# Kernel tuning notes

Measured on AMD Instinct MI355X. Metric: run time of the kernel, lower is better.

Reference implementation:

```python
import jax, jax.numpy as jnp
import numpy as np

D = 4096
B_BITS = 4
NUM_CENTROIDS = 2 ** B_BITS  # 16 uniform centroids in [-1, 1]
N_TOKENS = 8192


def setup_inputs() -> dict:
    key = jax.random.key(0)
    kx, kp = jax.random.split(key)
    x = jax.random.normal(kx, (N_TOKENS, D), dtype=jnp.float32)
    # Orthogonal rotation Pi via QR of a random Gaussian (matches torch.linalg.qr)
    rand_mat = jax.random.normal(kp, (D, D), dtype=jnp.float32)
    Pi, _ = jnp.linalg.qr(rand_mat)
    centroids = jnp.linspace(-1.0, 1.0, NUM_CENTROIDS, dtype=jnp.float32)
    return {"x": x, "Pi": Pi, "centroids": centroids}


def _quantize(y, centroids):
    # Centroids are uniformly spaced on [-1, 1]; nearest-centroid argmin has the
    # closed form below (identical result to the broadcast |y - c| argmin, without
    # materializing the O(N*d*2^b) distance tensor).
    n = centroids.shape[0]
    scale = (n - 1) * 0.5
    idx = jnp.clip(jnp.round((y + 1.0) * scale), 0, n - 1).astype(jnp.int32)
    return centroids[idx]


def reference(x, Pi, centroids):
    y = x @ Pi.T                      # [N, d] rotate into quantization basis
    y_q = _quantize(y, centroids)     # nearest uniform centroid
    x_tilde = y_q @ Pi                # rotate back
    return x_tilde
```

## Files before the change

### kernel.cpp

```cpp
#include <hip/hip_runtime.h>
#include <hip/hip_bf16.h>

#define DD 4096
#define NTOK 8192

using u16 = unsigned short;

typedef __attribute__((ext_vector_type(8))) short bfrag;
typedef __attribute__((ext_vector_type(4))) float ffrag;
typedef __attribute__((ext_vector_type(4))) float f32x4v;

__device__ __forceinline__ u16 f2bf(float f) {
  unsigned u = __float_as_uint(f);
  u += 0x7FFFu + ((u >> 16) & 1u);
  return (u16)(u >> 16);
}
__device__ __forceinline__ float bf2f(u16 u) {
  return __uint_as_float(((unsigned)u) << 16);
}

#define GLDS16(g, l)                                                  \
  __builtin_amdgcn_global_load_lds(                                   \
      (__attribute__((address_space(1))) const void*)(g),             \
      (__attribute__((address_space(3))) void*)(l), 16, 0, 0)

#define MEMFENCE() asm volatile("" ::: "memory")

__global__ void __launch_bounds__(256) split_bf16_kernel(
    const float* __restrict__ in, u16* __restrict__ hi,
    u16* __restrict__ lo, long n4) {
  long i = (long)blockIdx.x * blockDim.x + threadIdx.x;
  const long stride = (long)gridDim.x * blockDim.x;
  for (; i < n4; i += stride) {
    f32x4v v = reinterpret_cast<const f32x4v*>(in)[i];
    u16 h[4], l[4];
#pragma unroll
    for (int j = 0; j < 4; ++j) {
      float f = v[j];
      u16 hb = f2bf(f);
      h[j] = hb;
      l[j] = f2bf(f - bf2f(hb));
    }
    ushort4 hv, lv;
    hv.x = h[0]; hv.y = h[1]; hv.z = h[2]; hv.w = h[3];
    lv.x = l[0]; lv.y = l[1]; lv.z = l[2]; lv.w = l[3];
    reinterpret_cast<ushort4*>(hi)[i] = hv;
    reinterpret_cast<ushort4*>(lo)[i] = lv;
  }
}

__global__ void __launch_bounds__(256) transpose_bf16_kernel(
    const float* __restrict__ in, u16* __restrict__ out, int R, int C) {
  __shared__ u16 tile[64][65];
  const int bc = blockIdx.x << 6;
  const int br = blockIdx.y << 6;
  const int tc = threadIdx.x & 63;
  const int tr0 = threadIdx.x >> 6;
#pragma unroll
  for (int p = 0; p < 16; ++p) {
    int r = tr0 + (p << 2);
    tile[tc][r] = f2bf(in[(size_t)(br + r) * C + (bc + tc)]);
  }
  __syncthreads();
#pragma unroll
  for (int p = 0; p < 16; ++p) {
    int orow = tr0 + (p << 2);
    out[(size_t)(bc + orow) * R + (br + tc)] = tile[orow][tc];
  }
}

template <int NSEG, bool QUANT>
__global__ void __launch_bounds__(512, 2) gemm256_kernel(
    const u16* __restrict__ A0, const u16* __restrict__ A1,
    const u16* __restrict__ B0, const u16* __restrict__ B1,
    void* __restrict__ Cout, const float* __restrict__ cent,
    int M, int N) {
  constexpr int NT = NSEG * 64;
  __shared__ __align__(16) char SM[131072];
  __shared__ float clut[16];
  const int tid = threadIdx.x;
  if (QUANT && tid < 16) clut[tid] = cent[tid];

  const int nbn = N >> 8;
  const int nwg = (M >> 8) * nbn;
  int wg = blockIdx.x;
  wg = (wg & 7) * (nwg >> 3) + (wg >> 3);
  const int tm = (wg / nbn) << 8;
  const int tn = (wg % nbn) << 8;

  const int lane = tid & 63;
  const int wv = tid >> 6;
  const int wm = wv >> 2;
  const int wn = wv & 3;
  const int l15 = lane & 15;
  const int kslc = lane >> 4;
  const int cXor = (lane & 7) << 4;

  const size_t thrOff =
      (size_t)(wv * 8 + (lane >> 3)) * 4096 + 8 * ((lane & 7) ^ (lane >> 3));
  const int ldsThr = wv * 1024 + lane * 16;

  auto STAGE = [&](int h) {
    if (h >= 4 * NT) return;
    const int tau = h >> 2, idx = h & 3;
    const int b = tau & 1;
    const int seg = (NSEG == 3) ? (tau >> 6) : 0;
    const size_t ktE = (size_t)(tau & 63) * 64;
    const u16* src;
    char* lds;
    if (idx < 2) {
      const u16* bbase = (NSEG == 3 && seg == 2) ? B1 : B0;
      src = bbase + (size_t)(tn + idx * 128) * 4096 + ktE + thrOff;
      lds = SM + b * 65536 + 32768 + idx * 16384 + ldsThr;
    } else {
      const u16* abase = (NSEG == 3 && seg == 1) ? A1 : A0;
      src = abase + (size_t)(tm + (idx - 2) * 128) * 4096 + ktE + thrOff;
      lds = SM + b * 65536 + (idx - 2) * 16384 + ldsThr;
    }
    GLDS16(src, lds);
    GLDS16(src + 262144, lds + 8192);
  };

#define LDSA(b, f, s)                                                      \
  (*reinterpret_cast<const bfrag*>(                                        \
      SM + (b) * 65536 + wm * 16384 + (((f) * 16 + l15) << 7) +            \
      ((((s) << 6) | (kslc << 4)) ^ cXor)))
#define LDSB(b, f, s)                                                      \
  (*reinterpret_cast<const bfrag*>(                                        \
      SM + (b) * 65536 + 32768 + (wn >> 1) * 16384 +                       \
      ((((wn & 1) * 64) + (f) * 16 + l15) << 7) +                          \
      ((((s) << 6) | (kslc << 4)) ^ cXor)))

  ffrag acc[8][4];
#pragma unroll
  for (int m = 0; m < 8; ++m)
#pragma unroll
    for (int n = 0; n < 4; ++n) acc[m][n] = {0.f, 0.f, 0.f, 0.f};

#pragma unroll
  for (int h = 0; h < 7; ++h) STAGE(h);
  asm volatile("s_waitcnt vmcnt(6)" ::: "memory");
  MEMFENCE();
  __builtin_amdgcn_s_barrier();

  bfrag Af[8][2], Bf[4][2];

  for (int t = 0; t < NT; ++t) {
    const int b = t & 1;
    const int hb = 7 + 4 * t;
#pragma unroll
    for (int p = 0; p < 4; ++p) {
      if (p == 0) {
#pragma unroll
        for (int n = 0; n < 4; ++n) {
          Bf[n][0] = LDSB(b, n, 0);
          Bf[n][1] = LDSB(b, n, 1);
        }
#pragma unroll
        for (int m = 0; m < 4; ++m) {
          Af[m][0] = LDSA(b, m, 0);
          Af[m][1] = LDSA(b, m, 1);
        }
      } else if (p == 1) {
        Af[4][0] = LDSA(b, 4, 0); Af[4][1] = LDSA(b, 4, 1);
        Af[5][0] = LDSA(b, 5, 0); Af[5][1] = LDSA(b, 5, 1);
      } else if (p == 2) {
        Af[6][0] = LDSA(b, 6, 0); Af[6][1] = LDSA(b, 6, 1);
        Af[7][0] = LDSA(b, 7, 0); Af[7][1] = LDSA(b, 7, 1);
      }
      STAGE(hb + p);
      MEMFENCE();
      __builtin_amdgcn_s_barrier();
      asm volatile("s_waitcnt lgkmcnt(0)" ::: "memory");
      __builtin_amdgcn_sched_barrier(0);
      __builtin_amdgcn_s_setprio(1);
      {
        const int m0 = p * 2;
#pragma unroll
        for (int mm = 0; mm < 2; ++mm)
#pragma unroll
          for (int n = 0; n < 4; ++n) {
            acc[m0 + mm][n] = __builtin_amdgcn_mfma_f32_16x16x32_bf16(
                Af[m0 + mm][0], Bf[n][0], acc[m0 + mm][n], 0, 0, 0);
            acc[m0 + mm][n] = __builtin_amdgcn_mfma_f32_16x16x32_bf16(
                Af[m0 + mm][1], Bf[n][1], acc[m0 + mm][n], 0, 0, 0);
          }
      }
      __builtin_amdgcn_s_setprio(0);
      if (p == 3) {
        if (t == NT - 2)
          asm volatile("s_waitcnt vmcnt(0)" ::: "memory");
        else if (t < NT - 2)
          asm volatile("s_waitcnt vmcnt(6)" ::: "memory");
      }
      MEMFENCE();
      __builtin_amdgcn_s_barrier();
    }
  }

  const int r0 = tm + wm * 128 + kslc * 4;
  const int c0 = tn + wn * 64 + l15;
  if constexpr (QUANT) {
    u16* Y = reinterpret_cast<u16*>(Cout);
#pragma unroll
    for (int m = 0; m < 8; ++m)
#pragma unroll
      for (int n = 0; n < 4; ++n)
#pragma unroll
        for (int r = 0; r < 4; ++r) {
          float y = acc[m][n][r];
          float s = rintf((y + 1.0f) * 7.5f);
          int idx = (int)s;
          idx = idx < 0 ? 0 : (idx > 15 ? 15 : idx);
          Y[(size_t)(r0 + m * 16 + r) * N + (c0 + n * 16)] = f2bf(clut[idx]);
        }
  } else {
    float* Co = reinterpret_cast<float*>(Cout);
#pragma unroll
    for (int m = 0; m < 8; ++m)
#pragma unroll
      for (int n = 0; n < 4; ++n)
#pragma unroll
        for (int r = 0; r < 4; ++r)
          Co[(size_t)(r0 + m * 16 + r) * N + (c0 + n * 16)] = acc[m][n][r];
  }
#undef LDSA
#undef LDSB
}

extern "C" void kernel_launch(void* const* d_in, const int* in_sizes, int n_in,
                              void* d_out, int out_size, void* d_ws, size_t ws_size,
                              hipStream_t stream) {
  const float* x = (const float*)d_in[0];
  const float* Pi = (const float*)d_in[1];
  const float* cent = (const float*)d_in[2];
  float* out = (float*)d_out;

  const size_t MB = (size_t)1 << 20;
  if (ws_size < 288 * MB) return;

  char* ws = (char*)d_ws;
  u16* x_hi = (u16*)(ws + 0 * MB);
  u16* x_lo = (u16*)(ws + 64 * MB);
  u16* p_hi = (u16*)(ws + 128 * MB);
  u16* p_lo = (u16*)(ws + 160 * MB);
  u16* piT  = (u16*)(ws + 192 * MB);
  u16* yq   = (u16*)(ws + 224 * MB);

  split_bf16_kernel<<<2048, 256, 0, stream>>>(x, x_hi, x_lo, (long)NTOK * DD / 4);
  split_bf16_kernel<<<1024, 256, 0, stream>>>(Pi, p_hi, p_lo, (long)DD * DD / 4);
  transpose_bf16_kernel<<<dim3(DD / 64, DD / 64), 256, 0, stream>>>(Pi, piT, DD, DD);

  const int nwg = (NTOK / 256) * (DD / 256);
  gemm256_kernel<3, true><<<nwg, 512, 0, stream>>>(
      x_hi, x_lo, p_hi, p_lo, yq, cent, NTOK, DD);
  gemm256_kernel<1, false><<<nwg, 512, 0, stream>>>(
      yq, nullptr, piT, nullptr, out, nullptr, NTOK, DD);
}
```

Measured before the change: 1.078 ms.

## Restructure GEMM prefetch schedule: B two tiles ahead, A one ahead, smaller fragments

The GEMM main loop now prefetches B tiles two k-steps ahead and A tiles one step ahead, instead of using a uniform four-part staging sequence. Each quarter-iteration loads a single k-slice of fragments (4 A and 4 B), which shrinks the fragment register arrays to a quarter of their previous size. The vmcnt waits and prologue are adjusted to match, and the sched_barrier before the MFMA block is removed. The aim is to lower register pressure and spread global-to-LDS traffic more evenly. The trade-off is more frequent LDS fragment reloads, and the compiler now has more freedom to reorder around the MFMAs, which may hurt or help the schedule.

```diff
diff --git a/kernel.cpp b/kernel.cpp
--- a/kernel.cpp
+++ b/kernel.cpp
@@ -100,22 +100,22 @@
       (size_t)(wv * 8 + (lane >> 3)) * 4096 + 8 * ((lane & 7) ^ (lane >> 3));
   const int ldsThr = wv * 1024 + lane * 16;
 
-  auto STAGE = [&](int h) {
-    if (h >= 4 * NT) return;
-    const int tau = h >> 2, idx = h & 3;
+  auto STAGE = [&](int kind, int tau) {
+    if (tau >= NT) return;
     const int b = tau & 1;
     const int seg = (NSEG == 3) ? (tau >> 6) : 0;
     const size_t ktE = (size_t)(tau & 63) * 64;
     const u16* src;
     char* lds;
-    if (idx < 2) {
+    if (kind >= 2) {
       const u16* bbase = (NSEG == 3 && seg == 2) ? B1 : B0;
+      const int idx = kind - 2;
       src = bbase + (size_t)(tn + idx * 128) * 4096 + ktE + thrOff;
       lds = SM + b * 65536 + 32768 + idx * 16384 + ldsThr;
     } else {
       const u16* abase = (NSEG == 3 && seg == 1) ? A1 : A0;
-      src = abase + (size_t)(tm + (idx - 2) * 128) * 4096 + ktE + thrOff;
-      lds = SM + b * 65536 + (idx - 2) * 16384 + ldsThr;
+      src = abase + (size_t)(tm + kind * 128) * 4096 + ktE + thrOff;
+      lds = SM + b * 65536 + kind * 16384 + ldsThr;
     }
     GLDS16(src, lds);
     GLDS16(src + 262144, lds + 8192);
@@ -137,61 +137,45 @@
 #pragma unroll
     for (int n = 0; n < 4; ++n) acc[m][n] = {0.f, 0.f, 0.f, 0.f};
 
-#pragma unroll
-  for (int h = 0; h < 7; ++h) STAGE(h);
-  asm volatile("s_waitcnt vmcnt(6)" ::: "memory");
+  STAGE(0, 0); STAGE(1, 0); STAGE(2, 0); STAGE(3, 0);
+  STAGE(2, 1); STAGE(3, 1);
+  asm volatile("s_waitcnt vmcnt(4)" ::: "memory");
   MEMFENCE();
   __builtin_amdgcn_s_barrier();
 
-  bfrag Af[8][2], Bf[4][2];
+  bfrag Af[4], Bf[4];
 
   for (int t = 0; t < NT; ++t) {
     const int b = t & 1;
-    const int hb = 7 + 4 * t;
 #pragma unroll
     for (int p = 0; p < 4; ++p) {
-      if (p == 0) {
-#pragma unroll
-        for (int n = 0; n < 4; ++n) {
-          Bf[n][0] = LDSB(b, n, 0);
-          Bf[n][1] = LDSB(b, n, 1);
-        }
-#pragma unroll
-        for (int m = 0; m < 4; ++m) {
-          Af[m][0] = LDSA(b, m, 0);
-          Af[m][1] = LDSA(b, m, 1);
-        }
-      } else if (p == 1) {
-        Af[4][0] = LDSA(b, 4, 0); Af[4][1] = LDSA(b, 4, 1);
-        Af[5][0] = LDSA(b, 5, 0); Af[5][1] = LDSA(b, 5, 1);
-      } else if (p == 2) {
-        Af[6][0] = LDSA(b, 6, 0); Af[6][1] = LDSA(b, 6, 1);
-        Af[7][0] = LDSA(b, 7, 0); Af[7][1] = LDSA(b, 7, 1);
+      const int s = p >> 1;
+      const int mb = (p & 1) * 4;
+      if ((p & 1) == 0) {
+#pragma unroll
+        for (int n = 0; n < 4; ++n) Bf[n] = LDSB(b, n, s);
       }
-      STAGE(hb + p);
+#pragma unroll
+      for (int m = 0; m < 4; ++m) Af[m] = LDSA(b, mb + m, s);
+      if (p == 0) STAGE(0, t + 1);
+      else if (p == 1) STAGE(1, t + 1);
+      else if (p == 3) { STAGE(2, t + 2); STAGE(3, t + 2); }
       MEMFENCE();
       __builtin_amdgcn_s_barrier();
       asm volatile("s_waitcnt lgkmcnt(0)" ::: "memory");
-      __builtin_amdgcn_sched_barrier(0);
       __builtin_amdgcn_s_setprio(1);
-      {
-        const int m0 = p * 2;
-#pragma unroll
-        for (int mm = 0; mm < 2; ++mm)
-#pragma unroll
-          for (int n = 0; n < 4; ++n) {
-            acc[m0 + mm][n] = __builtin_amdgcn_mfma_f32_16x16x32_bf16(
-                Af[m0 + mm][0], Bf[n][0], acc[m0 + mm][n], 0, 0, 0);
-            acc[m0 + mm][n] = __builtin_amdgcn_mfma_f32_16x16x32_bf16(
-                Af[m0 + mm][1], Bf[n][1], acc[m0 + mm][n], 0, 0, 0);
-          }
-      }
+#pragma unroll
+      for (int m = 0; m < 4; ++m)
+#pragma unroll
+        for (int n = 0; n < 4; ++n)
+          acc[mb + m][n] = __builtin_amdgcn_mfma_f32_16x16x32_bf16(
+              Af[m], Bf[n], acc[mb + m][n], 0, 0, 0);
       __builtin_amdgcn_s_setprio(0);
       if (p == 3) {
         if (t == NT - 2)
           asm volatile("s_waitcnt vmcnt(0)" ::: "memory");
         else if (t < NT - 2)
-          asm volatile("s_waitcnt vmcnt(6)" ::: "memory");
+          asm volatile("s_waitcnt vmcnt(4)" ::: "memory");
       }
       MEMFENCE();
       __builtin_amdgcn_s_barrier();
```

Result: slower. 1.150 ms (+6.7%).
